# Optimization experiments

Hardware: AMD Instinct MI355X
Metric: run time of the kernel (lower is better)

Reference implementation:

```python
import jax, jax.numpy as jnp
import numpy as np


def _adder2d(x, w, stride, padding):
    """AdderNet 'convolution': out[b,o,i,j] = -sum_p |patch[b,p,i,j] - w[o,p]|.

    x: [B, C, H, W], w: [O, C, kh, kw]. Patches are extracted in (C, kh, kw)
    channel-major order, matching torch.nn.functional.unfold / w.reshape(O, -1).
    """
    O, C, kh, kw = w.shape
    patches = jax.lax.conv_general_dilated_patches(
        x, (kh, kw), (stride, stride), [(padding, padding), (padding, padding)])
    B, P, Ho, Wo = patches.shape  # P = C*kh*kw
    p = patches.reshape(B, P, Ho * Wo)
    wf = w.reshape(O, P)

    def per_out(wo):  # sequential over small O to avoid a [B,O,P,L] blowup
        return -jnp.sum(jnp.abs(p - wo[None, :, None]), axis=1)  # [B, L]

    out = jax.lax.map(per_out, wf)  # [O, B, L]
    return jnp.transpose(out, (1, 0, 2)).reshape(B, O, Ho, Wo)


def setup_inputs() -> dict:
    key = jax.random.key(0)
    ks = jax.random.split(key, 5)
    x = jax.random.normal(ks[0], (4096, 1, 28, 28), dtype=jnp.float32)
    w1 = jax.random.normal(ks[1], (16, 1, 3, 3), dtype=jnp.float32)
    w2 = jax.random.normal(ks[2], (32, 16, 3, 3), dtype=jnp.float32)
    w3 = jax.random.normal(ks[3], (16, 32, 3, 3), dtype=jnp.float32)
    w4 = jax.random.normal(ks[4], (10, 16, 3, 3), dtype=jnp.float32)
    return {"x": x, "w1": w1, "w2": w2, "w3": w3, "w4": w4}


def reference(x, w1, w2, w3, w4):
    h = x - 0.5
    h = jax.nn.relu((_adder2d(h, w1, 2, 0) + 10.0) / 4.0)   # [B,16,13,13]
    h = jax.nn.relu((_adder2d(h, w2, 2, 1) + 130.0) / 8.0)  # [B,32,7,7]
    h = jax.nn.relu((_adder2d(h, w3, 2, 1) + 280.0) / 16.0)  # [B,16,4,4]
    h = _adder2d(h, w4, 2, 0)                                # [B,10,1,1]
    h = h.reshape(h.shape[0], -1)                            # [B,10]
    return jax.nn.log_softmax(h, axis=1)
```

## Files before the change

kernel.cpp:

```cpp
#include <hip/hip_runtime.h>
#include <math.h>


#if defined(__has_builtin)
#if __has_builtin(__builtin_amdgcn_sad_u16)
#define HAS_SAD 1
#endif
#endif

__device__ __forceinline__ unsigned sadu16(unsigned a, unsigned b, unsigned acc) {
#ifdef HAS_SAD
  return __builtin_amdgcn_sad_u16(a, b, acc);
#else
  int al = (int)(a & 0xFFFFu), ah = (int)(a >> 16);
  int bl = (int)(b & 0xFFFFu), bh = (int)(b >> 16);
  return acc + (unsigned)(al > bl ? al - bl : bl - al)
             + (unsigned)(ah > bh ? ah - bh : bh - ah);
#endif
}

__device__ __forceinline__ unsigned quant(float v) {
  return (unsigned)fmaf(v, 1024.0f, 8192.5f);
}
__device__ __forceinline__ unsigned quantx(float v) {
  return (unsigned)fmaf(v, 1024.0f, 7680.5f);
}
__device__ __forceinline__ int imax(int a, int b) { return a > b ? a : b; }

#define QPAD 0x20002000u
#define A1STRIDE 19
#define A1PLANE 285

__global__ void adder_prep(const float* __restrict__ w1, const float* __restrict__ w2,
                           const float* __restrict__ w3, const float* __restrict__ w4,
                           unsigned* __restrict__ qw) {
  int k = blockIdx.x * 256 + threadIdx.x;
  if (k < 96) {
    int o = k / 6, r = k % 6, kh = r >> 1, h = r & 1;
    const float* p = w1 + o * 9 + kh * 3;
    qw[k] = h ? quant(p[2]) : (quant(p[0]) | (quant(p[1]) << 16));
  } else if (k < 2400) {
    int k2 = k - 96, m = k2 / 288, r = k2 % 288, o = r / 9, pk = r % 9;
    int s = o * 144 + 2 * m * 9 + pk;
    qw[k] = quant(w2[s]) | (quant(w2[s + 9]) << 16);
  } else if (k < 4704) {
    int k3 = k - 2400, m2 = k3 / 144, r = k3 % 144, o = r / 9, pk = r % 9;
    int s = o * 288 + 2 * m2 * 9 + pk;
    qw[k] = quant(w3[s]) | (quant(w3[s + 9]) << 16);
  } else if (k < 5424) {
    int k4 = k - 4704, m = k4 / 90, r = k4 % 90, o = r / 9, pk = r % 9;
    int s = o * 144 + 2 * m * 9 + pk;
    qw[k] = quant(w4[s]) | (quant(w4[s + 9]) << 16);
  }
}

__global__ __launch_bounds__(128, 4) void adder_main(
    const float* __restrict__ gx,
    const unsigned* __restrict__ qw,
    float* __restrict__ gout)
{
  __shared__ __align__(16) unsigned sA1[2280];
  __shared__ __align__(16) unsigned sA2[1296];

  const int t = threadIdx.x;
  const int l = t & 63;
  const int wu = __builtin_amdgcn_readfirstlane(t >> 6);
  const int b = blockIdx.x;
  const float* img = gx + (size_t)b * 784;

  for (int k = t; k < 448; k += 128) {
    int plane = k / 56, c = k % 56;
    int y, x;
    if (c < 15)      { y = 0;      x = c; }
    else if (c < 30) { y = 14;     x = c - 15; }
    else if (c < 43) { y = c - 29; x = 0; }
    else             { y = c - 42; x = 14; }
    sA1[plane * A1PLANE + y * A1STRIDE + x] = QPAD;
  }
  for (int k = t; k < 512; k += 128) {
    int plane = k >> 5, c = k & 31;
    int y, x;
    if (c < 9)       { y = 0; x = c; }
    else if (c < 18) { y = 8; x = c - 9; }
    else if (c < 25) { y = c - 17; x = 0; }
    else             { y = c - 24; x = 8; }
    sA2[plane * 81 + y * 9 + x] = QPAD;
  }

  if (l < 52) {
    const int i = l >> 2, jq = l & 3;
    unsigned r[3][5], mw[3][4];
#pragma unroll
    for (int kh = 0; kh < 3; ++kh) {
      const float* rp = img + (2 * i + kh) * 28 + 8 * jq;
      float4 A = *(const float4*)(rp);
      float4 B = *(const float4*)(rp + 4);
      float2 C = *(const float2*)(rp + 8);
      r[kh][0] = quantx(A.x) | (quantx(A.y) << 16);
      r[kh][1] = quantx(A.z) | (quantx(A.w) << 16);
      r[kh][2] = quantx(B.x) | (quantx(B.y) << 16);
      r[kh][3] = quantx(B.z) | (quantx(B.w) << 16);
      r[kh][4] = quantx(C.x) | (quantx(C.y) << 16);
#pragma unroll
      for (int c = 0; c < 4; ++c) mw[kh][c] = r[kh][c + 1] & 0xFFFFu;
    }
#pragma unroll 1
    for (int opp = 0; opp < 4; ++opp) {
      const int op = wu * 4 + opp;
      const unsigned* w = qw + op * 12;
      unsigned a0[4], a1[4];
#pragma unroll
      for (int jj = 0; jj < 4; ++jj) { a0[jj] = 0u; a1[jj] = 0u; }
#pragma unroll
      for (int kh = 0; kh < 3; ++kh) {
        unsigned wa01 = w[kh * 2], wa2 = w[kh * 2 + 1];
        unsigned wb01 = w[6 + kh * 2], wb2 = w[6 + kh * 2 + 1];
#pragma unroll
        for (int jj = 0; jj < 4; ++jj) {
          a0[jj] = sadu16(r[kh][jj], wa01, a0[jj]);
          a0[jj] = sadu16(mw[kh][jj], wa2, a0[jj]);
          a1[jj] = sadu16(r[kh][jj], wb01, a1[jj]);
          a1[jj] = sadu16(mw[kh][jj], wb2, a1[jj]);
        }
      }
      unsigned* dst = sA1 + op * A1PLANE + (i + 1) * A1STRIDE + 4 * jq + 1;
#pragma unroll
      for (int jj = 0; jj < 4; ++jj) {
        if (4 * jq + jj < 13) {
          int q0 = imax(10752 - (int)((a0[jj] + 2u) >> 2), 8192);
          int q1 = imax(10752 - (int)((a1[jj] + 2u) >> 2), 8192);
          dst[jj] = (unsigned)q0 | ((unsigned)q1 << 16);
        }
      }
    }
  }
  __syncthreads();

  if (l < 49) {
    const int i = l / 7, j = l % 7;
    unsigned acc[16];
#pragma unroll
    for (int o = 0; o < 16; ++o) acc[o] = 0u;
    const unsigned* qw2 = qw + 96 + wu * 144;
#pragma unroll 1
    for (int m = 0; m < 8; ++m) {
      const unsigned* plane = sA1 + m * A1PLANE + 2 * j;
      unsigned p[3][3];
#pragma unroll
      for (int kh = 0; kh < 3; ++kh)
#pragma unroll
        for (int c = 0; c < 3; ++c)
          p[kh][c] = plane[(2 * i + kh) * A1STRIDE + c];
      const unsigned* wm = qw2 + m * 288;
#pragma unroll
      for (int o = 0; o < 16; ++o) {
        const unsigned* w9 = wm + o * 9;
        unsigned a = acc[o];
#pragma unroll
        for (int kh = 0; kh < 3; ++kh)
#pragma unroll
          for (int c = 0; c < 3; ++c)
            a = sadu16(p[kh][c], w9[kh * 3 + c], a);
        acc[o] = a;
      }
    }
#pragma unroll
    for (int m2 = 0; m2 < 8; ++m2) {
      int q0 = imax(24832 - (int)((acc[2 * m2] + 4u) >> 3), 8192);
      int q1 = imax(24832 - (int)((acc[2 * m2 + 1] + 4u) >> 3), 8192);
      sA2[(wu * 8 + m2) * 81 + (i + 1) * 9 + (j + 1)] = (unsigned)q0 | ((unsigned)q1 << 16);
    }
  }
  __syncthreads();

  {
    const int pos = l & 15, g = l >> 4;
    const int i = pos >> 2, j = pos & 3;
    unsigned acc[8];
#pragma unroll
    for (int o = 0; o < 8; ++o) acc[o] = 0u;
    const unsigned* qw3 = qw + 2400 + wu * 72;
#pragma unroll 1
    for (int mm = 0; mm < 4; ++mm) {
      const int m2 = g * 4 + mm;
      const unsigned* plane = sA2 + m2 * 81 + 2 * j;
      unsigned p[3][3];
#pragma unroll
      for (int kh = 0; kh < 3; ++kh)
#pragma unroll
        for (int c = 0; c < 3; ++c)
          p[kh][c] = plane[(2 * i + kh) * 9 + c];
      const unsigned* ws = qw3 + m2 * 144;
#pragma unroll
      for (int oo = 0; oo < 8; ++oo) {
        const unsigned* w9 = ws + oo * 9;
        unsigned a = acc[oo];
#pragma unroll
        for (int kh = 0; kh < 3; ++kh)
#pragma unroll
          for (int c = 0; c < 3; ++c)
            a = sadu16(p[kh][c], w9[kh * 3 + c], a);
        acc[oo] = a;
      }
    }
#pragma unroll
    for (int oo = 0; oo < 8; ++oo)
      sA1[oo * 128 + g * 32 + wu * 16 + pos] = acc[oo];
  }
  __syncthreads();

  {
    const int m = t >> 4, pos = t & 15;
    const int ww = m >> 2;
    const int oo0 = 2 * m - ww * 8;
    unsigned s0 = 0u, s1 = 0u;
#pragma unroll
    for (int g = 0; g < 4; ++g) {
      s0 += sA1[oo0 * 128 + g * 32 + ww * 16 + pos];
      s1 += sA1[(oo0 + 1) * 128 + g * 32 + ww * 16 + pos];
    }
    int q0 = imax(26112 - (int)((s0 + 8u) >> 4), 8192);
    int q1 = imax(26112 - (int)((s1 + 8u) >> 4), 8192);
    sA1[1040 + m * 17 + pos] = (unsigned)q0 | ((unsigned)q1 << 16);
  }
  __syncthreads();

  if (t < 40) {
    const int o = t % 10, mq = t / 10;
    const unsigned* qw4 = qw + 4704;
    unsigned acc = 0u;
#pragma unroll
    for (int mm = 0; mm < 2; ++mm) {
      const int m = mq * 2 + mm;
      const unsigned* a3 = sA1 + 1040 + m * 17;
      const unsigned* w9 = qw4 + (m * 10 + o) * 9;
#pragma unroll
      for (int kh = 0; kh < 3; ++kh)
#pragma unroll
        for (int kw = 0; kw < 3; ++kw)
          acc = sadu16(a3[kh * 4 + kw], w9[kh * 3 + kw], acc);
    }
    sA1[1176 + t] = acc;
  }
  __syncthreads();
  if (t < 10) {
    unsigned s = sA1[1176 + t] + sA1[1186 + t] + sA1[1196 + t] + sA1[1206 + t];
    ((float*)sA1)[1216 + t] = -(float)s * (1.0f / 1024.0f);
  }
  __syncthreads();
  if (t < 10) {
    const float* lg = (const float*)sA1 + 1216;
    float mx = lg[0];
#pragma unroll
    for (int k = 1; k < 10; ++k) mx = fmaxf(mx, lg[k]);
    float sum = 0.0f;
#pragma unroll
    for (int k = 0; k < 10; ++k) sum += __expf(lg[k] - mx);
    gout[(size_t)b * 10 + t] = lg[t] - mx - __logf(sum);
  }
}

extern "C" void kernel_launch(void* const* d_in, const int* in_sizes, int n_in,
                              void* d_out, int out_size, void* d_ws, size_t ws_size,
                              hipStream_t stream) {
  const float* x  = (const float*)d_in[0];
  const float* w1 = (const float*)d_in[1];
  const float* w2 = (const float*)d_in[2];
  const float* w3 = (const float*)d_in[3];
  const float* w4 = (const float*)d_in[4];
  unsigned* qw = (unsigned*)d_ws;
  float* out = (float*)d_out;
  adder_prep<<<22, 256, 0, stream>>>(w1, w2, w3, w4, qw);
  adder_main<<<4096, 128, 0, stream>>>(x, qw, out);
}
```

Baseline: 108.9 us.

## Pad LDS rows against bank conflicts, prefetch patches, restructure layer-3 reduction

Shared-memory row offsets get an extra skew (y*19 + y/2, y*9 + y/2) and plane strides are padded to 288 and 85 to reduce LDS bank conflicts. Layers 2 and 3 now software-pipeline the next plane's 3x3 patch loads while computing the current one. Layer 3 is remapped so each thread owns one output pair over all 16 input planes, which removes the partial-sum buffer and one __syncthreads reduction stage. Launch bounds rise to 6 blocks per SM and the layer-1 loop is unrolled by 2, at the cost of more register pressure and serial work per thread in layer 3.

```diff
diff --git a/kernel.cpp b/kernel.cpp
--- a/kernel.cpp
+++ b/kernel.cpp
@@ -26,10 +26,10 @@
   return (unsigned)fmaf(v, 1024.0f, 7680.5f);
 }
 __device__ __forceinline__ int imax(int a, int b) { return a > b ? a : b; }
+__device__ __forceinline__ int yoff1(int y) { return y * 19 + (y >> 1); }
+__device__ __forceinline__ int yoff2(int y) { return y * 9 + (y >> 1); }
 
 #define QPAD 0x20002000u
-#define A1STRIDE 19
-#define A1PLANE 285
 
 __global__ void adder_prep(const float* __restrict__ w1, const float* __restrict__ w2,
                            const float* __restrict__ w3, const float* __restrict__ w4,
@@ -54,13 +54,13 @@
   }
 }
 
-__global__ __launch_bounds__(128, 4) void adder_main(
+__global__ __launch_bounds__(128, 6) void adder_main(
     const float* __restrict__ gx,
     const unsigned* __restrict__ qw,
     float* __restrict__ gout)
 {
-  __shared__ __align__(16) unsigned sA1[2280];
-  __shared__ __align__(16) unsigned sA2[1296];
+  __shared__ __align__(16) unsigned sA1[2304];
+  __shared__ __align__(16) unsigned sA2[1360];
 
   const int t = threadIdx.x;
   const int l = t & 63;
@@ -75,16 +75,7 @@
     else if (c < 30) { y = 14;     x = c - 15; }
     else if (c < 43) { y = c - 29; x = 0; }
     else             { y = c - 42; x = 14; }
-    sA1[plane * A1PLANE + y * A1STRIDE + x] = QPAD;
-  }
-  for (int k = t; k < 512; k += 128) {
-    int plane = k >> 5, c = k & 31;
-    int y, x;
-    if (c < 9)       { y = 0; x = c; }
-    else if (c < 18) { y = 8; x = c - 9; }
-    else if (c < 25) { y = c - 17; x = 0; }
-    else             { y = c - 24; x = 8; }
-    sA2[plane * 81 + y * 9 + x] = QPAD;
+    sA1[plane * 288 + yoff1(y) + x] = QPAD;
   }
 
   if (l < 52) {
@@ -104,7 +95,8 @@
 #pragma unroll
       for (int c = 0; c < 4; ++c) mw[kh][c] = r[kh][c + 1] & 0xFFFFu;
     }
-#pragma unroll 1
+    const int dbase = yoff1(i + 1) + 4 * jq + 1;
+#pragma unroll 2
     for (int opp = 0; opp < 4; ++opp) {
       const int op = wu * 4 + opp;
       const unsigned* w = qw + op * 12;
@@ -123,7 +115,7 @@
           a1[jj] = sadu16(mw[kh][jj], wb2, a1[jj]);
         }
       }
-      unsigned* dst = sA1 + op * A1PLANE + (i + 1) * A1STRIDE + 4 * jq + 1;
+      unsigned* dst = sA1 + op * 288 + dbase;
 #pragma unroll
       for (int jj = 0; jj < 4; ++jj) {
         if (4 * jq + jj < 13) {
@@ -136,21 +128,39 @@
   }
   __syncthreads();
 
+  for (int k = t; k < 512; k += 128) {
+    int plane = k >> 5, c = k & 31;
+    int y, x;
+    if (c < 9)       { y = 0; x = c; }
+    else if (c < 18) { y = 8; x = c - 9; }
+    else if (c < 25) { y = c - 17; x = 0; }
+    else             { y = c - 24; x = 8; }
+    sA2[plane * 85 + yoff2(y) + x] = QPAD;
+  }
+
   if (l < 49) {
     const int i = l / 7, j = l % 7;
     unsigned acc[16];
 #pragma unroll
     for (int o = 0; o < 16; ++o) acc[o] = 0u;
     const unsigned* qw2 = qw + 96 + wu * 144;
+    const unsigned* pb = sA1 + 39 * i + 2 * j;
+    const int K1o[3] = {0, 19, 39};
+    unsigned p[3][3];
+#pragma unroll
+    for (int kh = 0; kh < 3; ++kh)
+#pragma unroll
+      for (int c = 0; c < 3; ++c)
+        p[kh][c] = pb[K1o[kh] + c];
 #pragma unroll 1
     for (int m = 0; m < 8; ++m) {
-      const unsigned* plane = sA1 + m * A1PLANE + 2 * j;
-      unsigned p[3][3];
-#pragma unroll
-      for (int kh = 0; kh < 3; ++kh)
-#pragma unroll
-        for (int c = 0; c < 3; ++c)
-          p[kh][c] = plane[(2 * i + kh) * A1STRIDE + c];
+      unsigned pn[3][3];
+      const unsigned* pbn = pb + (((m + 1) & 7) * 288);
+#pragma unroll
+      for (int kh = 0; kh < 3; ++kh)
+#pragma unroll
+        for (int c = 0; c < 3; ++c)
+          pn[kh][c] = pbn[K1o[kh] + c];
       const unsigned* wm = qw2 + m * 288;
 #pragma unroll
       for (int o = 0; o < 16; ++o) {
@@ -163,65 +173,61 @@
             a = sadu16(p[kh][c], w9[kh * 3 + c], a);
         acc[o] = a;
       }
+#pragma unroll
+      for (int kh = 0; kh < 3; ++kh)
+#pragma unroll
+        for (int c = 0; c < 3; ++c)
+          p[kh][c] = pn[kh][c];
     }
 #pragma unroll
     for (int m2 = 0; m2 < 8; ++m2) {
       int q0 = imax(24832 - (int)((acc[2 * m2] + 4u) >> 3), 8192);
       int q1 = imax(24832 - (int)((acc[2 * m2 + 1] + 4u) >> 3), 8192);
-      sA2[(wu * 8 + m2) * 81 + (i + 1) * 9 + (j + 1)] = (unsigned)q0 | ((unsigned)q1 << 16);
+      sA2[(wu * 8 + m2) * 85 + yoff2(i + 1) + (j + 1)] = (unsigned)q0 | ((unsigned)q1 << 16);
     }
   }
   __syncthreads();
 
   {
-    const int pos = l & 15, g = l >> 4;
+    const int pos = l & 15, oq = l >> 4;
     const int i = pos >> 2, j = pos & 3;
-    unsigned acc[8];
-#pragma unroll
-    for (int o = 0; o < 8; ++o) acc[o] = 0u;
-    const unsigned* qw3 = qw + 2400 + wu * 72;
+    const int pr = wu * 4 + oq;
+    const unsigned* qw3 = qw + 2400 + pr * 18;
+    unsigned acc0 = 0u, acc1 = 0u;
+    const unsigned* pb = sA2 + 19 * i + 2 * j;
+    const int K2o[3] = {0, 9, 19};
+    unsigned p[3][3];
+#pragma unroll
+    for (int kh = 0; kh < 3; ++kh)
+#pragma unroll
+      for (int c = 0; c < 3; ++c)
+        p[kh][c] = pb[K2o[kh] + c];
 #pragma unroll 1
-    for (int mm = 0; mm < 4; ++mm) {
-      const int m2 = g * 4 + mm;
-      const unsigned* plane = sA2 + m2 * 81 + 2 * j;
-      unsigned p[3][3];
-#pragma unroll
-      for (int kh = 0; kh < 3; ++kh)
-#pragma unroll
-        for (int c = 0; c < 3; ++c)
-          p[kh][c] = plane[(2 * i + kh) * 9 + c];
-      const unsigned* ws = qw3 + m2 * 144;
-#pragma unroll
-      for (int oo = 0; oo < 8; ++oo) {
-        const unsigned* w9 = ws + oo * 9;
-        unsigned a = acc[oo];
-#pragma unroll
-        for (int kh = 0; kh < 3; ++kh)
-#pragma unroll
-          for (int c = 0; c < 3; ++c)
-            a = sadu16(p[kh][c], w9[kh * 3 + c], a);
-        acc[oo] = a;
-      }
-    }
-#pragma unroll
-    for (int oo = 0; oo < 8; ++oo)
-      sA1[oo * 128 + g * 32 + wu * 16 + pos] = acc[oo];
-  }
-  __syncthreads();
-
-  {
-    const int m = t >> 4, pos = t & 15;
-    const int ww = m >> 2;
-    const int oo0 = 2 * m - ww * 8;
-    unsigned s0 = 0u, s1 = 0u;
-#pragma unroll
-    for (int g = 0; g < 4; ++g) {
-      s0 += sA1[oo0 * 128 + g * 32 + ww * 16 + pos];
-      s1 += sA1[(oo0 + 1) * 128 + g * 32 + ww * 16 + pos];
-    }
-    int q0 = imax(26112 - (int)((s0 + 8u) >> 4), 8192);
-    int q1 = imax(26112 - (int)((s1 + 8u) >> 4), 8192);
-    sA1[1040 + m * 17 + pos] = (unsigned)q0 | ((unsigned)q1 << 16);
+    for (int m2 = 0; m2 < 16; ++m2) {
+      unsigned pn[3][3];
+      const unsigned* pbn = pb + (((m2 + 1) & 15) * 85);
+#pragma unroll
+      for (int kh = 0; kh < 3; ++kh)
+#pragma unroll
+        for (int c = 0; c < 3; ++c)
+          pn[kh][c] = pbn[K2o[kh] + c];
+      const unsigned* w18 = qw3 + m2 * 144;
+#pragma unroll
+      for (int kh = 0; kh < 3; ++kh)
+#pragma unroll
+        for (int c = 0; c < 3; ++c) {
+          acc0 = sadu16(p[kh][c], w18[kh * 3 + c], acc0);
+          acc1 = sadu16(p[kh][c], w18[9 + kh * 3 + c], acc1);
+        }
+#pragma unroll
+      for (int kh = 0; kh < 3; ++kh)
+#pragma unroll
+        for (int c = 0; c < 3; ++c)
+          p[kh][c] = pn[kh][c];
+    }
+    int q0 = imax(26112 - (int)((acc0 + 8u) >> 4), 8192);
+    int q1 = imax(26112 - (int)((acc1 + 8u) >> 4), 8192);
+    sA1[pr * 17 + pos] = (unsigned)q0 | ((unsigned)q1 << 16);
   }
   __syncthreads();
 
@@ -232,7 +238,7 @@
 #pragma unroll
     for (int mm = 0; mm < 2; ++mm) {
       const int m = mq * 2 + mm;
-      const unsigned* a3 = sA1 + 1040 + m * 17;
+      const unsigned* a3 = sA1 + m * 17;
       const unsigned* w9 = qw4 + (m * 10 + o) * 9;
 #pragma unroll
       for (int kh = 0; kh < 3; ++kh)
@@ -240,16 +246,16 @@
         for (int kw = 0; kw < 3; ++kw)
           acc = sadu16(a3[kh * 4 + kw], w9[kh * 3 + kw], acc);
     }
-    sA1[1176 + t] = acc;
+    sA1[200 + t] = acc;
   }
   __syncthreads();
   if (t < 10) {
-    unsigned s = sA1[1176 + t] + sA1[1186 + t] + sA1[1196 + t] + sA1[1206 + t];
-    ((float*)sA1)[1216 + t] = -(float)s * (1.0f / 1024.0f);
+    unsigned s = sA1[200 + t] + sA1[210 + t] + sA1[220 + t] + sA1[230 + t];
+    ((float*)sA1)[248 + t] = -(float)s * (1.0f / 1024.0f);
   }
   __syncthreads();
   if (t < 10) {
-    const float* lg = (const float*)sA1 + 1216;
+    const float* lg = (const float*)sA1 + 248;
     float mx = lg[0];
 #pragma unroll
     for (int k = 1; k < 10; ++k) mx = fmaxf(mx, lg[k]);
```

After: 110.7 us. Within noise of the previous version (+1.7%).
